# Kernel optimization log

Hardware: AMD Instinct MI355X
Metric: run time of the kernel (lower is better)

The kernel has to match this reference:

```python
import jax, jax.numpy as jnp
import numpy as np

B, T, D = 512, 200, 512

def setup_inputs() -> dict:
    key = jax.random.key(0)
    k1, k2, k3 = jax.random.split(key, 3)
    inputs = jax.random.normal(k1, (B, T, D), dtype=jnp.float32)
    # Keras 'uniform' initializer -> U(-0.05, 0.05)
    W = jax.random.uniform(k2, (T, T), minval=-0.05, maxval=0.05, dtype=jnp.float32)
    b = jax.random.uniform(k3, (T,), minval=-0.05, maxval=0.05, dtype=jnp.float32)
    return {"inputs": inputs, "W": W, "b": b}

def reference(inputs, W, b):
    # x = permute(inputs, (0,2,1)) -> [B, D, T]; scores over timestep axis
    # a = softmax(tanh(x @ W + b)) along last axis (T)
    scores = jnp.tanh(jnp.einsum('btd,ts->bds', inputs, W) + b)  # [B, D, T]
    a = jax.nn.softmax(scores, axis=-1)                           # softmax over T
    # permute back to [B, T, D], elementwise multiply, sum over T -> [B, D]
    out = jnp.einsum('bdt,btd->bd', a, inputs)
    return out
```

## Files before the change

kernel.cpp:

```cpp
#include <hip/hip_runtime.h>
#include <cstdint>
#include <cstddef>

#define B_DIM 512
#define T_DIM 200
#define D_DIM 512
#define NPAD  208
#define NKG   28
#define NT    13
#define KS_STEPS 7

typedef short  short8  __attribute__((ext_vector_type(8)));
typedef float  floatx4 __attribute__((ext_vector_type(4)));

__device__ __forceinline__ unsigned short f2bf(float f) {
  unsigned int u = __float_as_uint(f);
  u += 0x7fffu + ((u >> 16) & 1u);
  return (unsigned short)(u >> 16);
}
__device__ __forceinline__ float bf2f(unsigned short h) {
  return __uint_as_float(((unsigned int)h) << 16);
}

__global__ void prep_w_kernel(const float* __restrict__ W,
                              unsigned short* __restrict__ wf) {
  int idx = blockIdx.x * blockDim.x + threadIdx.x;
  if (idx >= NKG * 8 * NPAD) return;
  int k = idx / NPAD;
  int n = idx - k * NPAD;
  float v = (k < T_DIM && n < T_DIM) ? W[k * T_DIM + n] : 0.0f;
  wf[((size_t)(k >> 3) * NPAD + n) * 8 + (k & 7)] = f2bf(v);
}

__global__ __launch_bounds__(256, 4)
void attn_kernel(const float* __restrict__ X,
                 const unsigned short* __restrict__ wf,
                 const float* __restrict__ bias,
                 float* __restrict__ out) {
  __shared__ __align__(16) unsigned short Xa[4 * NKG * 16 * 8];

  const int tid  = threadIdx.x;
  const int wv   = tid >> 6;
  const int lane = tid & 63;
  const int l15  = lane & 15;
  const int g    = lane >> 4;

  const int gw = blockIdx.x * 4 + wv;
  const int bb = gw >> 5;
  const int d0 = (gw & 31) << 4;

  unsigned short* Xw = Xa + wv * (NKG * 16 * 8);
  const float* xbase = X + (size_t)bb * T_DIM * D_DIM + d0 + l15;

  float cur[8], nxt[8];
  {
    const float* p = xbase + (size_t)(g * 8) * D_DIM;
    #pragma unroll
    for (int j = 0; j < 8; ++j) cur[j] = p[(size_t)j * D_DIM];
  }
  #pragma unroll
  for (int ks = 0; ks < KS_STEPS; ++ks) {
    if (ks < 6) {
      if (ks < 5 || g == 0) {
        const float* p = xbase + (size_t)((ks + 1) * 32 + g * 8) * D_DIM;
        #pragma unroll
        for (int j = 0; j < 8; ++j) nxt[j] = p[(size_t)j * D_DIM];
      } else {
        #pragma unroll
        for (int j = 0; j < 8; ++j) nxt[j] = 0.0f;
      }
    }
    int4 w;
    w.x = (int)f2bf(cur[0]) | ((int)f2bf(cur[1]) << 16);
    w.y = (int)f2bf(cur[2]) | ((int)f2bf(cur[3]) << 16);
    w.z = (int)f2bf(cur[4]) | ((int)f2bf(cur[5]) << 16);
    w.w = (int)f2bf(cur[6]) | ((int)f2bf(cur[7]) << 16);
    *(int4*)&Xw[(((ks * 4 + g) * 16) + l15) * 8] = w;
    #pragma unroll
    for (int j = 0; j < 8; ++j) cur[j] = nxt[j];
  }

  floatx4 acc[NT];
  #pragma unroll
  for (int nt = 0; nt < NT; ++nt)
    acc[nt] = (floatx4){0.f, 0.f, 0.f, 0.f};

  #pragma unroll
  for (int ks = 0; ks < KS_STEPS; ++ks) {
    const int kg = ks * 4 + g;
    short8 a = *(const short8*)&Xw[((kg * 16) + l15) * 8];
    const unsigned short* wp = wf + ((size_t)kg * NPAD + l15) * 8;
    #pragma unroll
    for (int nt = 0; nt < NT; ++nt) {
      short8 bfr = *(const short8*)(wp + nt * 16 * 8);
      acc[nt] = __builtin_amdgcn_mfma_f32_16x16x32_bf16(a, bfr, acc[nt], 0, 0, 0);
    }
  }

  float part[4] = {0.f, 0.f, 0.f, 0.f};
  float rs[4]   = {0.f, 0.f, 0.f, 0.f};
  #pragma unroll
  for (int nt = 0; nt < NT; ++nt) {
    const int t = nt * 16 + l15;
    const bool valid = (t < T_DIM);
    const float bvn = valid ? bias[t] : 0.0f;
    const unsigned short* xp = &Xw[((t >> 3) * 16) * 8 + (t & 7)];
    #pragma unroll
    for (int r = 0; r < 4; ++r) {
      if (valid) {
        float z  = acc[nt][r] + bvn;
        float e  = __expf(2.0f * z);
        float th = 1.0f - __fdividef(2.0f, e + 1.0f);
        float p  = __expf(th);
        rs[r]   += p;
        const int m = g * 4 + r;
        part[r] += p * bf2f(xp[m * 8]);
      }
    }
  }
  #pragma unroll
  for (int off = 1; off <= 8; off <<= 1)
    #pragma unroll
    for (int r = 0; r < 4; ++r) {
      part[r] += __shfl_xor(part[r], off, 16);
      rs[r]   += __shfl_xor(rs[r],   off, 16);
    }

  if (l15 == 0) {
    #pragma unroll
    for (int r = 0; r < 4; ++r)
      out[(size_t)bb * D_DIM + d0 + g * 4 + r] = part[r] * __frcp_rn(rs[r]);
  }
}

extern "C" void kernel_launch(void* const* d_in, const int* in_sizes, int n_in,
                              void* d_out, int out_size, void* d_ws, size_t ws_size,
                              hipStream_t stream) {
  const float* X  = (const float*)d_in[0];
  const float* W  = (const float*)d_in[1];
  const float* bs = (const float*)d_in[2];
  float* out = (float*)d_out;
  unsigned short* wf = (unsigned short*)d_ws;

  const int wtot = NKG * 8 * NPAD;
  hipLaunchKernelGGL(prep_w_kernel, dim3((wtot + 255) / 256), dim3(256), 0, stream,
                     W, wf);
  hipLaunchKernelGGL(attn_kernel, dim3(4096), dim3(256), 0, stream,
                     X, wf, bs, out);
}
```

Baseline: 342.2 us.

## Cooperatively load X tile with float4 coalesced reads into shared memory

```diff
diff --git a/kernel.cpp b/kernel.cpp
--- a/kernel.cpp
+++ b/kernel.cpp
@@ -9,6 +9,7 @@
 #define NKG   28
 #define NT    13
 #define KS_STEPS 7
+#define SLICE 3208
 
 typedef short  short8  __attribute__((ext_vector_type(8)));
 typedef float  floatx4 __attribute__((ext_vector_type(4)));
@@ -32,12 +33,12 @@
   wf[((size_t)(k >> 3) * NPAD + n) * 8 + (k & 7)] = f2bf(v);
 }
 
-__global__ __launch_bounds__(256, 4)
+__global__ __launch_bounds__(256, 6)
 void attn_kernel(const float* __restrict__ X,
                  const unsigned short* __restrict__ wf,
                  const float* __restrict__ bias,
                  float* __restrict__ out) {
-  __shared__ __align__(16) unsigned short Xa[4 * NKG * 16 * 8];
+  __shared__ __align__(16) unsigned short Xa[4 * SLICE];
 
   const int tid  = threadIdx.x;
   const int wv   = tid >> 6;
@@ -45,40 +46,32 @@
   const int l15  = lane & 15;
   const int g    = lane >> 4;
 
-  const int gw = blockIdx.x * 4 + wv;
-  const int bb = gw >> 5;
-  const int d0 = (gw & 31) << 4;
+  const int bid  = blockIdx.x;
+  const int bb   = bid >> 3;
+  const int dblk = (bid & 7) << 6;
+  const int d0   = dblk + (wv << 4);
 
-  unsigned short* Xw = Xa + wv * (NKG * 16 * 8);
-  const float* xbase = X + (size_t)bb * T_DIM * D_DIM + d0 + l15;
-
-  float cur[8], nxt[8];
   {
-    const float* p = xbase + (size_t)(g * 8) * D_DIM;
+    const float* xb = X + (size_t)bb * (T_DIM * D_DIM) + dblk;
     #pragma unroll
-    for (int j = 0; j < 8; ++j) cur[j] = p[(size_t)j * D_DIM];
-  }
-  #pragma unroll
-  for (int ks = 0; ks < KS_STEPS; ++ks) {
-    if (ks < 6) {
-      if (ks < 5 || g == 0) {
-        const float* p = xbase + (size_t)((ks + 1) * 32 + g * 8) * D_DIM;
-        #pragma unroll
-        for (int j = 0; j < 8; ++j) nxt[j] = p[(size_t)j * D_DIM];
-      } else {
-        #pragma unroll
-        for (int j = 0; j < 8; ++j) nxt[j] = 0.0f;
+    for (int it = 0; it < 13; ++it) {
+      int i = it * 256 + tid;
+      if (i < 3200) {
+        int t  = i >> 4;
+        int c4 = i & 15;
+        float4 v = *(const float4*)(xb + (size_t)t * D_DIM + (c4 << 2));
+        unsigned short* dst = Xa + (c4 >> 2) * SLICE
+                            + ((t >> 3) * 16 + ((c4 & 3) << 2)) * 8 + (t & 7);
+        dst[0]  = f2bf(v.x);
+        dst[8]  = f2bf(v.y);
+        dst[16] = f2bf(v.z);
+        dst[24] = f2bf(v.w);
       }
     }
-    int4 w;
-    w.x = (int)f2bf(cur[0]) | ((int)f2bf(cur[1]) << 16);
-    w.y = (int)f2bf(cur[2]) | ((int)f2bf(cur[3]) << 16);
-    w.z = (int)f2bf(cur[4]) | ((int)f2bf(cur[5]) << 16);
-    w.w = (int)f2bf(cur[6]) | ((int)f2bf(cur[7]) << 16);
-    *(int4*)&Xw[(((ks * 4 + g) * 16) + l15) * 8] = w;
-    #pragma unroll
-    for (int j = 0; j < 8; ++j) cur[j] = nxt[j];
   }
+  __syncthreads();
+
+  unsigned short* Xw = Xa + wv * SLICE;
 
   floatx4 acc[NT];
   #pragma unroll
@@ -88,7 +81,9 @@
   #pragma unroll
   for (int ks = 0; ks < KS_STEPS; ++ks) {
     const int kg = ks * 4 + g;
-    short8 a = *(const short8*)&Xw[((kg * 16) + l15) * 8];
+    short8 a = (short8){0, 0, 0, 0, 0, 0, 0, 0};
+    if (ks < 6 || g == 0)
+      a = *(const short8*)&Xw[(kg * 16 + l15) * 8];
     const unsigned short* wp = wf + ((size_t)kg * NPAD + l15) * 8;
     #pragma unroll
     for (int nt = 0; nt < NT; ++nt) {
```

New measurement: 413.2 us. 1.21x slower.
